# Kernel optimization log

Measured on AMD Instinct MI355X. Metric: run time of the kernel, lower is better.

The kernel has to match this reference:

```python
import jax, jax.numpy as jnp
import numpy as np

N = 100000   # nodes (single node type 'A')
C = 256      # hidden_channels
OUT = 128    # out_channels
E_RAND = 300000  # random edges; total E = N + E_RAND = 400000
LN_EPS = 1e-5


def _linear_params(key, in_c, out_c):
    kw, kb = jax.random.split(key)
    bound = 1.0 / np.sqrt(in_c)
    W = jax.random.uniform(kw, (out_c, in_c), minval=-bound, maxval=bound, dtype=jnp.float32)
    b = jax.random.uniform(kb, (out_c,), minval=-bound, maxval=bound, dtype=jnp.float32)
    return W, b


def _edges(key):
    # guarantee every node appears in both rows -> unique()/remap in the torch
    # code is the identity, so the subgraph equals the full graph
    k0, k1 = jax.random.split(key)
    base = jnp.arange(N, dtype=jnp.int64)
    row0 = jnp.concatenate([base, jax.random.randint(k0, (E_RAND,), 0, N, dtype=jnp.int64)])
    row1 = jnp.concatenate([base, jax.random.randint(k1, (E_RAND,), 0, N, dtype=jnp.int64)])
    return jnp.stack([row0, row1])


def setup_inputs() -> dict:
    key = jax.random.key(0)
    ks = jax.random.split(key, 12)
    x = jax.random.normal(ks[0], (N, C), dtype=jnp.float32)
    edge_index_r0 = _edges(ks[1])
    edge_index_r1 = _edges(ks[2])
    wl0, bl0 = _linear_params(ks[3], C, C)
    w00, b00 = _linear_params(ks[4], C, C)
    w10, b10 = _linear_params(ks[5], C, C)
    wl1, bl1 = _linear_params(ks[6], C, C)
    w01, b01 = _linear_params(ks[7], C, C)
    w11, b11 = _linear_params(ks[8], C, C)
    Wout, bout = _linear_params(ks[9], C, OUT)
    return dict(
        x=x, edge_index_r0=edge_index_r0, edge_index_r1=edge_index_r1,
        wl0=wl0, bl0=bl0, w00=w00, b00=b00, w10=w10, b10=b10,
        gate0=jnp.float32(0.5), lns0=jnp.ones((C,), jnp.float32), lnb0=jnp.zeros((C,), jnp.float32),
        wl1=wl1, bl1=bl1, w01=w01, b01=b01, w11=w11, b11=b11,
        gate1=jnp.float32(0.5), lns1=jnp.ones((C,), jnp.float32), lnb1=jnp.zeros((C,), jnp.float32),
        Wout=Wout, bout=bout,
    )


def _metapath_layer(x0, h, ei, wl, bl, w0, b0, w1, b1, gate, lns, lnb):
    n = h.shape[0]
    src, dst = ei[0], ei[1]
    # PyG flow='target_to_source', aggr='add': message x_j = h[edge_index[1]],
    # scatter-added at edge_index[0]
    agg = jax.ops.segment_sum(h[dst], src, num_segments=n)
    # original code normalizes by bincount of edge_index[1] (kept faithfully)
    deg = jax.ops.segment_sum(jnp.ones_like(dst, dtype=h.dtype), dst, num_segments=n)
    agg = agg / jnp.clip(deg, 1.0)[:, None]
    g = jax.nn.sigmoid(gate)
    out = (agg @ wl.T + bl) + (1.0 - g) * (h @ w0.T + b0) + g * (x0 @ w1.T + b1)
    out = jax.nn.relu(out)
    mu = out.mean(-1, keepdims=True)
    var = out.var(-1, keepdims=True)
    out = (out - mu) / jnp.sqrt(var + LN_EPS) * lns + lnb
    return out  # dropout is identity in eval mode


def reference(x, edge_index_r0, edge_index_r1,
              wl0, bl0, w00, b00, w10, b10, gate0, lns0, lnb0,
              wl1, bl1, w01, b01, w11, b11, gate1, lns1, lnb1,
              Wout, bout):
    x0 = jax.lax.stop_gradient(x)  # x0_dict is detached in the torch code
    h = x
    # metapath is processed in reverse: conv index 1 first, then conv index 0
    h = _metapath_layer(x0, h, edge_index_r1, wl1, bl1, w01, b01, w11, b11, gate1, lns1, lnb1)
    h = _metapath_layer(x0, h, edge_index_r0, wl0, bl0, w00, b00, w10, b10, gate0, lns0, lnb0)
    return h @ Wout.T + bout
```

## Files before the change

### kernel.cpp

```cpp
#include <hip/hip_runtime.h>

typedef unsigned short u16;
typedef unsigned int   u32;

typedef __attribute__((ext_vector_type(8))) __bf16 bf16x8;
typedef __attribute__((ext_vector_type(8))) unsigned short u16x8;
typedef __attribute__((ext_vector_type(4))) float  f32x4;

#define C      256
#define OUTC   128
#define LN_EPS 1e-5f

__device__ __forceinline__ float bf2f(u16 u) {
    u32 i = ((u32)u) << 16; float f; __builtin_memcpy(&f, &i, 4); return f;
}
__device__ __forceinline__ u16 f2bf(float f) {
    u32 i; __builtin_memcpy(&i, &f, 4);
    u32 r = (i + 0x7FFFu + ((i >> 16) & 1u)) >> 16;
    return (u16)r;
}
__device__ __forceinline__ void load_lds16(const void* g, void* l) {
    __builtin_amdgcn_global_load_lds((const __attribute__((address_space(1))) u32*)g,
                                     (__attribute__((address_space(3))) u32*)l, 16, 0, 0);
}
__device__ __forceinline__ int swz(int row) { return (row + (row >> 2)) & 3; }

#define PREP_BLK 1408
__global__ void prep_combo(const float* wl0, const float* w00, const float* w10,
                           const float* bl0, const float* b00, const float* b10,
                           const float* gate0,
                           const float* wl1, const float* w01, const float* w11,
                           const float* bl1, const float* b01, const float* b11,
                           const float* gate1,
                           const float* Wout, const float* x,
                           u16* __restrict__ WcatA, u16* __restrict__ WcatB,
                           u16* __restrict__ Woutb, float* __restrict__ bcat,
                           u16* __restrict__ xb, size_t n8)
{
    if (blockIdx.x >= PREP_BLK) {
        size_t i = ((size_t)(blockIdx.x - PREP_BLK) * 256 + threadIdx.x);
        if (i >= n8) return;
        const float* p = x + i * 8;
        float4 v0 = *(const float4*)p;
        float4 v1 = *(const float4*)(p + 4);
        u16x8 o;
        o[0] = f2bf(v0.x); o[1] = f2bf(v0.y); o[2] = f2bf(v0.z); o[3] = f2bf(v0.w);
        o[4] = f2bf(v1.x); o[5] = f2bf(v1.y); o[6] = f2bf(v1.z); o[7] = f2bf(v1.w);
        *(u16x8*)(xb + i * 8) = o;
        return;
    }
    int idx = blockIdx.x * 256 + threadIdx.x;
    float gA = 1.f / (1.f + expf(-gate1[0]));
    float gB = 1.f / (1.f + expf(-gate0[0]));
    if (idx < 256 * 512) {
        int n = idx >> 9, k = idx & 511;
        float v;
        if (k < 256) v = wl1[n * 256 + k];
        else         v = (1.f - gA) * w01[n * 256 + (k - 256)] + gA * w11[n * 256 + (k - 256)];
        WcatA[idx] = f2bf(v);
    } else if (idx < 256 * 512 + 256 * 768) {
        int j = idx - 256 * 512;
        int n = j / 768, k = j - n * 768;
        float v;
        if (k < 256)      v = wl0[n * 256 + k];
        else if (k < 512) v = (1.f - gB) * w00[n * 256 + (k - 256)];
        else              v = gB * w10[n * 256 + (k - 512)];
        WcatB[j] = f2bf(v);
    } else {
        int j = idx - (256 * 512 + 256 * 768);
        if (j < OUTC * C) Woutb[j] = f2bf(Wout[j]);
    }
    if (idx < 512) {
        int nn = idx & 255;
        if (idx < 256) bcat[idx] = bl1[nn] + (1.f - gA) * b01[nn] + gA * b11[nn];
        else           bcat[idx] = bl0[nn] + (1.f - gB) * b00[nn] + gB * b10[nn];
    }
}

__global__ void count_edges2(const int* __restrict__ ei1, const int* __restrict__ ei0,
                             int* __restrict__ cnt1, int* __restrict__ deg1,
                             int* __restrict__ cnt0, int* __restrict__ deg0,
                             int E, int Nn, int ebg)
{
    int b = blockIdx.x;
    const int* ei; int *cnt, *deg;
    if (b < ebg) { ei = ei1; cnt = cnt1; deg = deg1; }
    else         { b -= ebg; ei = ei0; cnt = cnt0; deg = deg0; }
    int idx = b * 256 + threadIdx.x;
    if (idx >= E) return;
    int s = ei[idx], d = ei[E + idx];
    if ((unsigned)s >= (unsigned)Nn || (unsigned)d >= (unsigned)Nn) return;
    atomicAdd(cnt + s, 1);
    atomicAdd(deg + d, 1);
}

__global__ void block_sums2(const int* __restrict__ cnt1, const int* __restrict__ cnt0,
                            int* __restrict__ parts1, int* __restrict__ parts0,
                            int n, int nblk)
{
    int b = blockIdx.x;
    const int* counts; int* partials;
    if (b < nblk) { counts = cnt1; partials = parts1; }
    else          { b -= nblk; counts = cnt0; partials = parts0; }
    int i = b * 256 + threadIdx.x;
    int v = (i < n) ? counts[i] : 0;
    #pragma unroll
    for (int off = 32; off; off >>= 1) v += __shfl_down(v, off, 64);
    __shared__ int ws[4];
    if ((threadIdx.x & 63) == 0) ws[threadIdx.x >> 6] = v;
    __syncthreads();
    if (threadIdx.x == 0) partials[b] = ws[0] + ws[1] + ws[2] + ws[3];
}

__global__ void scan_partials2(int* __restrict__ parts1, int* __restrict__ parts0, int nblk)
{
    int* partials = blockIdx.x ? parts0 : parts1;
    __shared__ int buf[1024];
    int tid = threadIdx.x;
    int v = (tid < nblk) ? partials[tid] : 0;
    buf[tid] = v; __syncthreads();
    for (int off = 1; off < 1024; off <<= 1) {
        int t = (tid >= off) ? buf[tid - off] : 0;
        __syncthreads();
        buf[tid] += t;
        __syncthreads();
    }
    if (tid < nblk) partials[tid] = buf[tid] - v;
}

__global__ void make_offsets2(int* __restrict__ cnt1, int* __restrict__ cnt0,
                              const int* __restrict__ parts1, const int* __restrict__ parts0,
                              int* __restrict__ off1a, int* __restrict__ off0a,
                              int n, int nblk)
{
    int b = blockIdx.x;
    int* counts_cursor; const int* partials; int* offsets;
    if (b < nblk) { counts_cursor = cnt1; partials = parts1; offsets = off1a; }
    else          { b -= nblk; counts_cursor = cnt0; partials = parts0; offsets = off0a; }
    __shared__ int buf[256];
    int i = b * 256 + threadIdx.x;
    int cnt = (i < n) ? counts_cursor[i] : 0;
    buf[threadIdx.x] = cnt; __syncthreads();
    for (int off = 1; off < 256; off <<= 1) {
        int t = (threadIdx.x >= off) ? buf[threadIdx.x - off] : 0;
        __syncthreads();
        buf[threadIdx.x] += t;
        __syncthreads();
    }
    int off = partials[b] + buf[threadIdx.x] - cnt;
    if (i < n) {
        offsets[i] = off;
        counts_cursor[i] = off;
        if (i == n - 1) offsets[n] = off + cnt;
    }
}

__global__ void fill_edges2(const int* __restrict__ ei1, const int* __restrict__ ei0,
                            int* __restrict__ cur1, int* __restrict__ cur0,
                            int* __restrict__ ed1, int* __restrict__ ed0,
                            int E, int Nn, int ebg)
{
    int b = blockIdx.x;
    const int* ei; int *cursor, *edgedst;
    if (b < ebg) { ei = ei1; cursor = cur1; edgedst = ed1; }
    else         { b -= ebg; ei = ei0; cursor = cur0; edgedst = ed0; }
    int idx = b * 256 + threadIdx.x;
    if (idx >= E) return;
    int s = ei[idx], d = ei[E + idx];
    if ((unsigned)s >= (unsigned)Nn || (unsigned)d >= (unsigned)Nn) return;
    int p = atomicAdd(cursor + s, 1);
    edgedst[p] = d;
}

__global__ __launch_bounds__(256) void gather_kernel(
    const int* __restrict__ offsets, const int* __restrict__ edgedst,
    const int* __restrict__ degcnt, const u16* __restrict__ h,
    u16* __restrict__ aggb, int Nn)
{
    int node = blockIdx.x * 4 + (threadIdx.x >> 6);
    if (node >= Nn) return;
    int lane = threadIdx.x & 63;
    int half = lane >> 5, l5 = lane & 31;
    int beg = offsets[node], end = offsets[node + 1];
    float a0[8] = {}, a1[8] = {};
    int p = beg;
    for (; p + 3 < end; p += 4) {
        int d0 = edgedst[p + half];
        int d1 = edgedst[p + 2 + half];
        u16x8 v0 = *(const u16x8*)(h + (size_t)d0 * C + l5 * 8);
        u16x8 v1 = *(const u16x8*)(h + (size_t)d1 * C + l5 * 8);
        #pragma unroll
        for (int j = 0; j < 8; ++j) { a0[j] += bf2f(v0[j]); a1[j] += bf2f(v1[j]); }
    }
    if (p + 1 < end) {
        int d0 = edgedst[p + half];
        u16x8 v0 = *(const u16x8*)(h + (size_t)d0 * C + l5 * 8);
        #pragma unroll
        for (int j = 0; j < 8; ++j) a0[j] += bf2f(v0[j]);
        p += 2;
    }
    if (p < end && half == 0) {
        int d0 = edgedst[p];
        u16x8 v0 = *(const u16x8*)(h + (size_t)d0 * C + l5 * 8);
        #pragma unroll
        for (int j = 0; j < 8; ++j) a1[j] += bf2f(v0[j]);
    }
    float inv = 1.0f / fmaxf((float)degcnt[node], 1.0f);
    u16x8 o;
    #pragma unroll
    for (int j = 0; j < 8; ++j) {
        float s = a0[j] + a1[j];
        s += __shfl_xor(s, 32);
        o[j] = f2bf(s * inv);
    }
    if (half == 0)
        *(u16x8*)(aggb + (size_t)node * C + l5 * 8) = o;
}

template <int NSEG>
__global__ __launch_bounds__(512, 2) void layer_gemm8(
    const u16* __restrict__ s0, const u16* __restrict__ s1, const u16* __restrict__ s2,
    const u16* __restrict__ W,
    const float* __restrict__ bcat,
    const float* __restrict__ lns, const float* __restrict__ lnb,
    u16* __restrict__ Hout, int Nnodes)
{
    constexpr int WK = NSEG * 256;
    constexpr int T  = NSEG * 4;

    extern __shared__ char smem[];
    u16*   A_e    = (u16*)smem;
    u16*   B_e    = (u16*)(smem + 65536);
    float* lnpart = (float*)(smem + 131072);

    const int tid  = threadIdx.x;
    const int wave = tid >> 6, lane = tid & 63;
    const int wave_m = wave & 1, wave_n = wave >> 1;
    const int q = lane >> 4, l15 = lane & 15;
    const int m0 = blockIdx.x * 256;

    size_t a_goff[2], b_goff[2];
    int ldso[2];
    #pragma unroll
    for (int i = 0; i < 2; ++i) {
        int o = i * 8192 + wave * 1024 + lane * 16;
        int g = o >> 7, slot = (o >> 4) & 7;
        int bc = slot ^ (g & 7);
        int r = 2 * g + (bc >> 2), c = bc & 3;
        int node = m0 + r; if (node >= Nnodes) node = Nnodes - 1;
        a_goff[i] = (size_t)node * C + c * 8;
        b_goff[i] = (size_t)r * WK + c * 8;
        ldso[i]   = i * 8192 + wave * 1024;
    }

    int aoffE[8], boffE[4];
    #pragma unroll
    for (int j = 0; j < 8; ++j) {
        int r = wave_m * 128 + j * 16 + l15;
        aoffE[j] = (r >> 1) * 64 + (((((r & 1) << 2) | q) ^ ((r >> 1) & 7)) << 3);
    }
    #pragma unroll
    for (int f = 0; f < 4; ++f) {
        int r = wave_n * 64 + f * 16 + l15;
        boffE[f] = (r >> 1) * 64 + (((((r & 1) << 2) | q) ^ ((r >> 1) & 7)) << 3);
    }

    f32x4 acc[8][4] = {};

    auto stA = [&](int buf, int kh, int t) {
        const u16* sp = (t < 4) ? s0 : ((NSEG == 2 || t < 8) ? s1 : s2);
        const u16* base = sp + ((t & 3) << 6) + (kh << 5);
        #pragma unroll
        for (int i = 0; i < 2; ++i)
            load_lds16(base + a_goff[i], (char*)A_e + buf * 32768 + kh * 16384 + ldso[i]);
    };
    auto stB = [&](int buf, int kh, int t) {
        const u16* base = W + (t << 6) + (kh << 5);
        #pragma unroll
        for (int i = 0; i < 2; ++i)
            load_lds16(base + b_goff[i], (char*)B_e + buf * 32768 + kh * 16384 + ldso[i]);
    };

#define LDA(DST, BASE, MH) \
    _Pragma("unroll") for (int j = 0; j < 4; ++j) \
        DST[j] = *(const bf16x8*)((BASE) + aoffE[(MH) * 4 + j]);
#define LDB(DST, BASE) \
    _Pragma("unroll") for (int f = 0; f < 4; ++f) \
        DST[f] = *(const bf16x8*)((BASE) + boffE[f]);
#define MFMA16(MH, AF, BF) \
    _Pragma("unroll") for (int j = 0; j < 4; ++j) \
        _Pragma("unroll") for (int f = 0; f < 4; ++f) \
            acc[(MH) * 4 + j][f] = __builtin_amdgcn_mfma_f32_16x16x32_bf16( \
                AF[j], BF[f], acc[(MH) * 4 + j][f], 0, 0, 0);
#define SBAR()  asm volatile("s_barrier" ::: "memory")

    stA(0, 0, 0); stB(0, 0, 0); stA(0, 1, 0); stB(0, 1, 0);

    int cur = 0;
    for (int t = 0; t < T - 1; ++t, cur ^= 1) {
        const u16* Ac = A_e + cur * 16384;
        const u16* Bc = B_e + cur * 16384;
        const int nxt = cur ^ 1;
        bf16x8 af[4], bfr[4];
        stA(nxt, 0, t + 1);
        asm volatile("s_waitcnt vmcnt(6)" ::: "memory");
        SBAR();
        __builtin_amdgcn_sched_barrier(0);
        LDB(bfr, Bc); LDA(af, Ac, 0);
        __builtin_amdgcn_s_setprio(1);
        MFMA16(0, af, bfr);
        __builtin_amdgcn_s_setprio(0);
        SBAR();
        LDA(af, Ac, 1);
        stB(nxt, 0, t + 1);
        SBAR();
        __builtin_amdgcn_s_setprio(1);
        MFMA16(1, af, bfr);
        __builtin_amdgcn_s_setprio(0);
        SBAR();
        stA(nxt, 1, t + 1);
        asm volatile("s_waitcnt vmcnt(6)" ::: "memory");
        SBAR();
        __builtin_amdgcn_sched_barrier(0);
        LDB(bfr, Bc + 8192); LDA(af, Ac + 8192, 0);
        __builtin_amdgcn_s_setprio(1);
        MFMA16(0, af, bfr);
        __builtin_amdgcn_s_setprio(0);
        SBAR();
        LDA(af, Ac + 8192, 1);
        stB(nxt, 1, t + 1);
        SBAR();
        __builtin_amdgcn_s_setprio(1);
        MFMA16(1, af, bfr);
        __builtin_amdgcn_s_setprio(0);
        SBAR();
    }
    {
        const u16* Ac = A_e + cur * 16384;
        const u16* Bc = B_e + cur * 16384;
        bf16x8 af[4], bfr[4];
        asm volatile("s_waitcnt vmcnt(4)" ::: "memory");
        SBAR();
        __builtin_amdgcn_sched_barrier(0);
        LDB(bfr, Bc); LDA(af, Ac, 0);
        __builtin_amdgcn_s_setprio(1);
        MFMA16(0, af, bfr);
        __builtin_amdgcn_s_setprio(0);
        SBAR();
        LDA(af, Ac, 1);
        SBAR();
        __builtin_amdgcn_s_setprio(1);
        MFMA16(1, af, bfr);
        __builtin_amdgcn_s_setprio(0);
        SBAR();
        asm volatile("s_waitcnt vmcnt(0)" ::: "memory");
        SBAR();
        __builtin_amdgcn_sched_barrier(0);
        LDB(bfr, Bc + 8192); LDA(af, Ac + 8192, 0);
        __builtin_amdgcn_s_setprio(1);
        MFMA16(0, af, bfr);
        __builtin_amdgcn_s_setprio(0);
        SBAR();
        LDA(af, Ac + 8192, 1);
        SBAR();
        __builtin_amdgcn_s_setprio(1);
        MFMA16(1, af, bfr);
        __builtin_amdgcn_s_setprio(0);
        SBAR();
    }

    float bias[4], lsc[4], lbi[4];
    #pragma unroll
    for (int f = 0; f < 4; ++f) {
        int n = wave_n * 64 + f * 16 + l15;
        bias[f] = bcat[n]; lsc[f] = lns[n]; lbi[f] = lnb[n];
    }
    #pragma unroll
    for (int t8 = 0; t8 < 8; ++t8)
        #pragma unroll
        for (int r = 0; r < 4; ++r) {
            float p = 0.f, pp = 0.f;
            #pragma unroll
            for (int f = 0; f < 4; ++f) {
                float v = acc[t8][f][r] + bias[f];
                v = fmaxf(v, 0.f);
                acc[t8][f][r] = v;
                p += v; pp += v * v;
            }
            #pragma unroll
            for (int off = 1; off < 16; off <<= 1) {
                p  += __shfl_xor(p,  off, 16);
                pp += __shfl_xor(pp, off, 16);
            }
            if (l15 == 0) {
                int row = wave_m * 128 + t8 * 16 + q * 4 + r;
                lnpart[row * 8 + wave_n * 2 + 0] = p;
                lnpart[row * 8 + wave_n * 2 + 1] = pp;
            }
        }
    __syncthreads();
    #pragma unroll
    for (int t8 = 0; t8 < 8; ++t8)
        #pragma unroll
        for (int r = 0; r < 4; ++r) {
            int row = wave_m * 128 + t8 * 16 + q * 4 + r;
            int node = m0 + row;
            if (node < Nnodes) {
                float S1 = lnpart[row * 8 + 0] + lnpart[row * 8 + 2]
                         + lnpart[row * 8 + 4] + lnpart[row * 8 + 6];
                float S2 = lnpart[row * 8 + 1] + lnpart[row * 8 + 3]
                         + lnpart[row * 8 + 5] + lnpart[row * 8 + 7];
                float mean = S1 * (1.f / 256.f);
                float var  = fmaxf(S2 * (1.f / 256.f) - mean * mean, 0.f);
                float rstd = rsqrtf(var + LN_EPS);
                u16* op = Hout + (size_t)node * C;
                #pragma unroll
                for (int f = 0; f < 4; ++f) {
                    int n = wave_n * 64 + f * 16 + l15;
                    op[n] = f2bf((acc[t8][f][r] - mean) * rstd * lsc[f] + lbi[f]);
                }
            }
        }
#undef LDA
#undef LDB
#undef MFMA16
#undef SBAR
}

__global__ __launch_bounds__(512, 4) void final_gemm(
    const u16* __restrict__ A, const u16* __restrict__ W,
    const float* __restrict__ bout, float* __restrict__ out, int Nnodes)
{
    __shared__ u16 Alds[2][128 * 32];
    __shared__ u16 Blds[2][128 * 32];

    const int tid = threadIdx.x;
    const int wave = tid >> 6, lane = tid & 63;
    const int wave_m = wave & 1, wave_n = wave >> 1;
    const int q = lane >> 4, l15 = lane & 15;
    const int m0 = blockIdx.x * 128;

    const int srow = (wave << 4) + (lane >> 2);
    int anode = m0 + srow; if (anode >= Nnodes) anode = Nnodes - 1;
    const int asc = (lane & 3) ^ swz(srow);
    const size_t a_goff = (size_t)anode * C + asc * 8;
    const int a_lo = wave << 9;

    const int bsc = (lane & 3) ^ swz(srow);
    const u16* bgp = W + srow * C + bsc * 8;
    const int b_lo = wave << 9;

    int aoff[4], boff[2];
    #pragma unroll
    for (int t = 0; t < 4; ++t) {
        int ar = wave_m * 64 + t * 16 + l15;
        aoff[t] = ar * 32 + ((q ^ swz(ar)) << 3);
    }
    #pragma unroll
    for (int f = 0; f < 2; ++f) {
        int br = wave_n * 32 + f * 16 + l15;
        boff[f] = br * 32 + ((q ^ swz(br)) << 3);
    }

    f32x4 acc[4][2] = {};

    auto stage = [&](int b, int kt) {
        int k0 = kt << 5;
        load_lds16(A + a_goff + k0, &Alds[b][a_lo]);
        load_lds16(bgp + k0, &Blds[b][b_lo]);
    };
    auto compute = [&](const u16* __restrict__ Ab, const u16* __restrict__ Bb) {
        bf16x8 af[4], bfr[2];
        #pragma unroll
        for (int t = 0; t < 4; ++t) af[t]  = *(const bf16x8*)(Ab + aoff[t]);
        #pragma unroll
        for (int f = 0; f < 2; ++f) bfr[f] = *(const bf16x8*)(Bb + boff[f]);
        #pragma unroll
        for (int t = 0; t < 4; ++t)
            #pragma unroll
            for (int f = 0; f < 2; ++f)
                acc[t][f] = __builtin_amdgcn_mfma_f32_16x16x32_bf16(af[t], bfr[f], acc[t][f], 0, 0, 0);
    };

    stage(0, 0);
    stage(1, 1);
    for (int kt = 0; kt < 6; kt += 2) {
        asm volatile("s_waitcnt vmcnt(2)" ::: "memory");
        __builtin_amdgcn_s_barrier();
        __builtin_amdgcn_sched_barrier(0);
        compute(&Alds[0][0], &Blds[0][0]);
        __builtin_amdgcn_sched_barrier(0);
        __builtin_amdgcn_s_barrier();
        stage(0, kt + 2);
        asm volatile("s_waitcnt vmcnt(2)" ::: "memory");
        __builtin_amdgcn_s_barrier();
        __builtin_amdgcn_sched_barrier(0);
        compute(&Alds[1][0], &Blds[1][0]);
        __builtin_amdgcn_sched_barrier(0);
        __builtin_amdgcn_s_barrier();
        stage(1, kt + 3);
    }
    asm volatile("s_waitcnt vmcnt(2)" ::: "memory");
    __builtin_amdgcn_s_barrier();
    __builtin_amdgcn_sched_barrier(0);
    compute(&Alds[0][0], &Blds[0][0]);
    asm volatile("s_waitcnt vmcnt(0)" ::: "memory");
    __builtin_amdgcn_s_barrier();
    __builtin_amdgcn_sched_barrier(0);
    compute(&Alds[1][0], &Blds[1][0]);

    float bias[2];
    #pragma unroll
    for (int f = 0; f < 2; ++f) bias[f] = bout[wave_n * 32 + f * 16 + l15];
    #pragma unroll
    for (int t = 0; t < 4; ++t)
        #pragma unroll
        for (int r = 0; r < 4; ++r) {
            int row = wave_m * 64 + t * 16 + q * 4 + r;
            int node = m0 + row;
            if (node < Nnodes) {
                float* op = out + (size_t)node * OUTC;
                #pragma unroll
                for (int f = 0; f < 2; ++f) {
                    int n = wave_n * 32 + f * 16 + l15;
                    op[n] = acc[t][f][r] + bias[f];
                }
            }
        }
}

extern "C" void kernel_launch(void* const* d_in, const int* in_sizes, int n_in,
                              void* d_out, int out_size, void* d_ws, size_t ws_size,
                              hipStream_t stream)
{
    const float* x    = (const float*)d_in[0];
    const int*   ei0  = (const int*)d_in[1];
    const int*   ei1  = (const int*)d_in[2];
    const float* wl0  = (const float*)d_in[3];
    const float* bl0  = (const float*)d_in[4];
    const float* w00  = (const float*)d_in[5];
    const float* b00  = (const float*)d_in[6];
    const float* w10  = (const float*)d_in[7];
    const float* b10  = (const float*)d_in[8];
    const float* gate0= (const float*)d_in[9];
    const float* lns0 = (const float*)d_in[10];
    const float* lnb0 = (const float*)d_in[11];
    const float* wl1  = (const float*)d_in[12];
    const float* bl1  = (const float*)d_in[13];
    const float* w01  = (const float*)d_in[14];
    const float* b01  = (const float*)d_in[15];
    const float* w11  = (const float*)d_in[16];
    const float* b11  = (const float*)d_in[17];
    const float* gate1= (const float*)d_in[18];
    const float* lns1 = (const float*)d_in[19];
    const float* lnb1 = (const float*)d_in[20];
    const float* Wout = (const float*)d_in[21];
    const float* bout = (const float*)d_in[22];

    const int N = in_sizes[0] / C;
    const int E = in_sizes[1] / 2;

    char* w = (char*)d_ws;
    u16*   WcatA = (u16*)w;   w += (size_t)256 * 512 * 2;
    u16*   WcatB = (u16*)w;   w += (size_t)256 * 768 * 2;
    u16*   Woutb = (u16*)w;   w += (size_t)OUTC * C * 2;
    float* bcat  = (float*)w; w += 4096;
    int*   cnt1  = (int*)w;   w += (size_t)N * 4;
    int*   deg1  = (int*)w;   w += (size_t)N * 4;
    int*   cnt0  = (int*)w;   w += (size_t)N * 4;
    int*   deg0  = (int*)w;   w += (size_t)N * 4;
    int*   off1  = (int*)w;   w += (((size_t)(N + 1) * 4) + 255) & ~255ull;
    int*   off0  = (int*)w;   w += (((size_t)(N + 1) * 4) + 255) & ~255ull;
    int*   parts1= (int*)w;   w += 4096;
    int*   parts0= (int*)w;   w += 4096;
    int*   ed1   = (int*)w;   w += (size_t)E * 4;
    int*   ed0   = (int*)w;   w += (size_t)E * 4;
    u16*   xb    = (u16*)w;   w += (size_t)N * C * 2;
    u16*   aggb  = (u16*)w;   w += (size_t)N * C * 2;
    u16*   h1    = (u16*)w;   w += (size_t)N * C * 2;

    const int eb_grid = (E + 255) / 256;
    const int nblk    = (N + 255) / 256;
    const int gt_grid = (N + 3) / 4;
    const int gm_grid = (N + 127) / 128;
    const int gm8     = (N + 255) / 256;
    const size_t n8   = (size_t)N * C / 8;
    const int xc_blk  = (int)((n8 + 255) / 256);
    const size_t lds8 = 139264;
    u16* h2 = (u16*)d_out;

    hipMemsetAsync(cnt1, 0, (size_t)4 * N * 4, stream);
    prep_combo<<<PREP_BLK + xc_blk, 256, 0, stream>>>(
        wl0, w00, w10, bl0, b00, b10, gate0,
        wl1, w01, w11, bl1, b01, b11, gate1,
        Wout, x, WcatA, WcatB, Woutb, bcat, xb, n8);

    count_edges2 <<<2 * eb_grid, 256, 0, stream>>>(ei1, ei0, cnt1, deg1, cnt0, deg0, E, N, eb_grid);
    block_sums2  <<<2 * nblk, 256, 0, stream>>>(cnt1, cnt0, parts1, parts0, N, nblk);
    scan_partials2<<<2, 1024, 0, stream>>>(parts1, parts0, nblk);
    make_offsets2<<<2 * nblk, 256, 0, stream>>>(cnt1, cnt0, parts1, parts0, off1, off0, N, nblk);
    fill_edges2  <<<2 * eb_grid, 256, 0, stream>>>(ei1, ei0, cnt1, cnt0, ed1, ed0, E, N, eb_grid);

    gather_kernel<<<gt_grid, 256, 0, stream>>>(off1, ed1, deg1, xb, aggb, N);
    layer_gemm8<2><<<gm8, 512, lds8, stream>>>(aggb, xb, nullptr, WcatA, bcat,
                                               lns1, lnb1, h1, N);

    gather_kernel<<<gt_grid, 256, 0, stream>>>(off0, ed0, deg0, h1, aggb, N);
    layer_gemm8<3><<<gm8, 512, lds8, stream>>>(aggb, h1, xb, WcatB, bcat + C,
                                               lns0, lnb0, h2, N);

    final_gemm<<<gm_grid, 512, 0, stream>>>(h2, Woutb, bout, (float*)d_out, N);
}
```

Before: 541.0 us.

## Fuse output projection into second layer GEMM and trim main-loop barriers

The second layer GEMM now writes its layer-normalized bf16 rows into swizzled LDS and runs the 256x128 output projection in the epilogue, reading Wout straight from global memory. This removes the separate final_gemm launch and the round trip of h2 through global memory. The main K loop also issues A and B stages together and waits once per half, which drops several s_barriers. In exchange the fused epilogue adds serial MFMA work after the main loop, and the fewer barriers assume LDS reads and writes do not race.

```diff
diff --git a/kernel.cpp b/kernel.cpp
--- a/kernel.cpp
+++ b/kernel.cpp
@@ -23,7 +23,6 @@
     __builtin_amdgcn_global_load_lds((const __attribute__((address_space(1))) u32*)g,
                                      (__attribute__((address_space(3))) u32*)l, 16, 0, 0);
 }
-__device__ __forceinline__ int swz(int row) { return (row + (row >> 2)) & 3; }
 
 #define PREP_BLK 1408
 __global__ void prep_combo(const float* wl0, const float* w00, const float* w10,
@@ -217,13 +216,15 @@
         *(u16x8*)(aggb + (size_t)node * C + l5 * 8) = o;
 }
 
-template <int NSEG>
+template <int NSEG, bool FUSE>
 __global__ __launch_bounds__(512, 2) void layer_gemm8(
     const u16* __restrict__ s0, const u16* __restrict__ s1, const u16* __restrict__ s2,
     const u16* __restrict__ W,
     const float* __restrict__ bcat,
     const float* __restrict__ lns, const float* __restrict__ lnb,
-    u16* __restrict__ Hout, int Nnodes)
+    u16* __restrict__ Hout,
+    const u16* __restrict__ WoutB, const float* __restrict__ boutp,
+    float* __restrict__ outp, int Nnodes)
 {
     constexpr int WK = NSEG * 256;
     constexpr int T  = NSEG * 4;
@@ -232,6 +233,7 @@
     u16*   A_e    = (u16*)smem;
     u16*   B_e    = (u16*)(smem + 65536);
     float* lnpart = (float*)(smem + 131072);
+    u16*   h2l    = (u16*)smem;
 
     const int tid  = threadIdx.x;
     const int wave = tid >> 6, lane = tid & 63;
@@ -302,34 +304,28 @@
         const u16* Bc = B_e + cur * 16384;
         const int nxt = cur ^ 1;
         bf16x8 af[4], bfr[4];
-        stA(nxt, 0, t + 1);
-        asm volatile("s_waitcnt vmcnt(6)" ::: "memory");
+        stA(nxt, 0, t + 1); stB(nxt, 0, t + 1);
+        asm volatile("s_waitcnt vmcnt(8)" ::: "memory");
         SBAR();
         __builtin_amdgcn_sched_barrier(0);
         LDB(bfr, Bc); LDA(af, Ac, 0);
         __builtin_amdgcn_s_setprio(1);
         MFMA16(0, af, bfr);
         __builtin_amdgcn_s_setprio(0);
-        SBAR();
         LDA(af, Ac, 1);
-        stB(nxt, 0, t + 1);
-        SBAR();
         __builtin_amdgcn_s_setprio(1);
         MFMA16(1, af, bfr);
         __builtin_amdgcn_s_setprio(0);
         SBAR();
-        stA(nxt, 1, t + 1);
-        asm volatile("s_waitcnt vmcnt(6)" ::: "memory");
+        stA(nxt, 1, t + 1); stB(nxt, 1, t + 1);
+        asm volatile("s_waitcnt vmcnt(8)" ::: "memory");
         SBAR();
         __builtin_amdgcn_sched_barrier(0);
         LDB(bfr, Bc + 8192); LDA(af, Ac + 8192, 0);
         __builtin_amdgcn_s_setprio(1);
         MFMA16(0, af, bfr);
         __builtin_amdgcn_s_setprio(0);
-        SBAR();
         LDA(af, Ac + 8192, 1);
-        stB(nxt, 1, t + 1);
-        SBAR();
         __builtin_amdgcn_s_setprio(1);
         MFMA16(1, af, bfr);
         __builtin_amdgcn_s_setprio(0);
@@ -346,9 +342,7 @@
         __builtin_amdgcn_s_setprio(1);
         MFMA16(0, af, bfr);
         __builtin_amdgcn_s_setprio(0);
-        SBAR();
         LDA(af, Ac, 1);
-        SBAR();
         __builtin_amdgcn_s_setprio(1);
         MFMA16(1, af, bfr);
         __builtin_amdgcn_s_setprio(0);
@@ -360,13 +354,10 @@
         __builtin_amdgcn_s_setprio(1);
         MFMA16(0, af, bfr);
         __builtin_amdgcn_s_setprio(0);
-        SBAR();
         LDA(af, Ac + 8192, 1);
-        SBAR();
         __builtin_amdgcn_s_setprio(1);
         MFMA16(1, af, bfr);
         __builtin_amdgcn_s_setprio(0);
-        SBAR();
     }
 
     float bias[4], lsc[4], lbi[4];
@@ -405,14 +396,21 @@
         for (int r = 0; r < 4; ++r) {
             int row = wave_m * 128 + t8 * 16 + q * 4 + r;
             int node = m0 + row;
-            if (node < Nnodes) {
-                float S1 = lnpart[row * 8 + 0] + lnpart[row * 8 + 2]
-                         + lnpart[row * 8 + 4] + lnpart[row * 8 + 6];
-                float S2 = lnpart[row * 8 + 1] + lnpart[row * 8 + 3]
-                         + lnpart[row * 8 + 5] + lnpart[row * 8 + 7];
-                float mean = S1 * (1.f / 256.f);
-                float var  = fmaxf(S2 * (1.f / 256.f) - mean * mean, 0.f);
-                float rstd = rsqrtf(var + LN_EPS);
+            float S1 = lnpart[row * 8 + 0] + lnpart[row * 8 + 2]
+                     + lnpart[row * 8 + 4] + lnpart[row * 8 + 6];
+            float S2 = lnpart[row * 8 + 1] + lnpart[row * 8 + 3]
+                     + lnpart[row * 8 + 5] + lnpart[row * 8 + 7];
+            float mean = S1 * (1.f / 256.f);
+            float var  = fmaxf(S2 * (1.f / 256.f) - mean * mean, 0.f);
+            float rstd = rsqrtf(var + LN_EPS);
+            if constexpr (FUSE) {
+                #pragma unroll
+                for (int f = 0; f < 4; ++f) {
+                    int n = wave_n * 64 + f * 16 + l15;
+                    u16 hv = f2bf((acc[t8][f][r] - mean) * rstd * lsc[f] + lbi[f]);
+                    h2l[row * 256 + (((n >> 3) ^ (row & 7)) << 3) + (n & 7)] = hv;
+                }
+            } else if (node < Nnodes) {
                 u16* op = Hout + (size_t)node * C;
                 #pragma unroll
                 for (int f = 0; f < 4; ++f) {
@@ -421,112 +419,49 @@
                 }
             }
         }
+
+    if constexpr (FUSE) {
+        __syncthreads();
+        f32x4 acc2[8][2] = {};
+        for (int kt = 0; kt < 8; ++kt) {
+            bf16x8 bw[2];
+            #pragma unroll
+            for (int f = 0; f < 2; ++f) {
+                int n = wave_n * 32 + f * 16 + l15;
+                bw[f] = *(const bf16x8*)(WoutB + (size_t)n * 256 + kt * 32 + q * 8);
+            }
+            #pragma unroll
+            for (int t8 = 0; t8 < 8; ++t8) {
+                int row = wave_m * 128 + t8 * 16 + l15;
+                bf16x8 a = *(const bf16x8*)(h2l + row * 256
+                                            + ((((kt << 2) | q) ^ (row & 7)) << 3));
+                #pragma unroll
+                for (int f = 0; f < 2; ++f)
+                    acc2[t8][f] = __builtin_amdgcn_mfma_f32_16x16x32_bf16(
+                        a, bw[f], acc2[t8][f], 0, 0, 0);
+            }
+        }
+        float b2[2];
+        #pragma unroll
+        for (int f = 0; f < 2; ++f) b2[f] = boutp[wave_n * 32 + f * 16 + l15];
+        #pragma unroll
+        for (int t8 = 0; t8 < 8; ++t8)
+            #pragma unroll
+            for (int r = 0; r < 4; ++r) {
+                int row = wave_m * 128 + t8 * 16 + q * 4 + r;
+                int node = m0 + row;
+                if (node < Nnodes) {
+                    float* op = outp + (size_t)node * OUTC;
+                    #pragma unroll
+                    for (int f = 0; f < 2; ++f)
+                        op[wave_n * 32 + f * 16 + l15] = acc2[t8][f][r] + b2[f];
+                }
+            }
+    }
 #undef LDA
 #undef LDB
 #undef MFMA16
 #undef SBAR
-}
-
-__global__ __launch_bounds__(512, 4) void final_gemm(
-    const u16* __restrict__ A, const u16* __restrict__ W,
-    const float* __restrict__ bout, float* __restrict__ out, int Nnodes)
-{
-    __shared__ u16 Alds[2][128 * 32];
-    __shared__ u16 Blds[2][128 * 32];
-
-    const int tid = threadIdx.x;
-    const int wave = tid >> 6, lane = tid & 63;
-    const int wave_m = wave & 1, wave_n = wave >> 1;
-    const int q = lane >> 4, l15 = lane & 15;
-    const int m0 = blockIdx.x * 128;
-
-    const int srow = (wave << 4) + (lane >> 2);
-    int anode = m0 + srow; if (anode >= Nnodes) anode = Nnodes - 1;
-    const int asc = (lane & 3) ^ swz(srow);
-    const size_t a_goff = (size_t)anode * C + asc * 8;
-    const int a_lo = wave << 9;
-
-    const int bsc = (lane & 3) ^ swz(srow);
-    const u16* bgp = W + srow * C + bsc * 8;
-    const int b_lo = wave << 9;
-
-    int aoff[4], boff[2];
-    #pragma unroll
-    for (int t = 0; t < 4; ++t) {
-        int ar = wave_m * 64 + t * 16 + l15;
-        aoff[t] = ar * 32 + ((q ^ swz(ar)) << 3);
-    }
-    #pragma unroll
-    for (int f = 0; f < 2; ++f) {
-        int br = wave_n * 32 + f * 16 + l15;
-        boff[f] = br * 32 + ((q ^ swz(br)) << 3);
-    }
-
-    f32x4 acc[4][2] = {};
-
-    auto stage = [&](int b, int kt) {
-        int k0 = kt << 5;
-        load_lds16(A + a_goff + k0, &Alds[b][a_lo]);
-        load_lds16(bgp + k0, &Blds[b][b_lo]);
-    };
-    auto compute = [&](const u16* __restrict__ Ab, const u16* __restrict__ Bb) {
-        bf16x8 af[4], bfr[2];
-        #pragma unroll
-        for (int t = 0; t < 4; ++t) af[t]  = *(const bf16x8*)(Ab + aoff[t]);
-        #pragma unroll
-        for (int f = 0; f < 2; ++f) bfr[f] = *(const bf16x8*)(Bb + boff[f]);
-        #pragma unroll
-        for (int t = 0; t < 4; ++t)
-            #pragma unroll
-            for (int f = 0; f < 2; ++f)
-                acc[t][f] = __builtin_amdgcn_mfma_f32_16x16x32_bf16(af[t], bfr[f], acc[t][f], 0, 0, 0);
-    };
-
-    stage(0, 0);
-    stage(1, 1);
-    for (int kt = 0; kt < 6; kt += 2) {
-        asm volatile("s_waitcnt vmcnt(2)" ::: "memory");
-        __builtin_amdgcn_s_barrier();
-        __builtin_amdgcn_sched_barrier(0);
-        compute(&Alds[0][0], &Blds[0][0]);
-        __builtin_amdgcn_sched_barrier(0);
-        __builtin_amdgcn_s_barrier();
-        stage(0, kt + 2);
-        asm volatile("s_waitcnt vmcnt(2)" ::: "memory");
-        __builtin_amdgcn_s_barrier();
-        __builtin_amdgcn_sched_barrier(0);
-        compute(&Alds[1][0], &Blds[1][0]);
-        __builtin_amdgcn_sched_barrier(0);
-        __builtin_amdgcn_s_barrier();
-        stage(1, kt + 3);
-    }
-    asm volatile("s_waitcnt vmcnt(2)" ::: "memory");
-    __builtin_amdgcn_s_barrier();
-    __builtin_amdgcn_sched_barrier(0);
-    compute(&Alds[0][0], &Blds[0][0]);
-    asm volatile("s_waitcnt vmcnt(0)" ::: "memory");
-    __builtin_amdgcn_s_barrier();
-    __builtin_amdgcn_sched_barrier(0);
-    compute(&Alds[1][0], &Blds[1][0]);
-
-    float bias[2];
-    #pragma unroll
-    for (int f = 0; f < 2; ++f) bias[f] = bout[wave_n * 32 + f * 16 + l15];
-    #pragma unroll
-    for (int t = 0; t < 4; ++t)
-        #pragma unroll
-        for (int r = 0; r < 4; ++r) {
-            int row = wave_m * 64 + t * 16 + q * 4 + r;
-            int node = m0 + row;
-            if (node < Nnodes) {
-                float* op = out + (size_t)node * OUTC;
-                #pragma unroll
-                for (int f = 0; f < 2; ++f) {
-                    int n = wave_n * 32 + f * 16 + l15;
-                    op[n] = acc[t][f][r] + bias[f];
-                }
-            }
-        }
 }
 
 extern "C" void kernel_launch(void* const* d_in, const int* in_sizes, int n_in,
@@ -582,12 +517,10 @@
     const int eb_grid = (E + 255) / 256;
     const int nblk    = (N + 255) / 256;
     const int gt_grid = (N + 3) / 4;
-    const int gm_grid = (N + 127) / 128;
     const int gm8     = (N + 255) / 256;
     const size_t n8   = (size_t)N * C / 8;
     const int xc_blk  = (int)((n8 + 255) / 256);
     const size_t lds8 = 139264;
-    u16* h2 = (u16*)d_out;
 
     hipMemsetAsync(cnt1, 0, (size_t)4 * N * 4, stream);
     prep_combo<<<PREP_BLK + xc_blk, 256, 0, stream>>>(
@@ -602,12 +535,12 @@
     fill_edges2  <<<2 * eb_grid, 256, 0, stream>>>(ei1, ei0, cnt1, cnt0, ed1, ed0, E, N, eb_grid);
 
     gather_kernel<<<gt_grid, 256, 0, stream>>>(off1, ed1, deg1, xb, aggb, N);
-    layer_gemm8<2><<<gm8, 512, lds8, stream>>>(aggb, xb, nullptr, WcatA, bcat,
-                                               lns1, lnb1, h1, N);
+    layer_gemm8<2, false><<<gm8, 512, lds8, stream>>>(aggb, xb, nullptr, WcatA, bcat,
+                                                      lns1, lnb1, h1,
+                                                      nullptr, nullptr, nullptr, N);
 
     gather_kernel<<<gt_grid, 256, 0, stream>>>(off0, ed0, deg0, h1, aggb, N);
-    layer_gemm8<3><<<gm8, 512, lds8, stream>>>(aggb, h1, xb, WcatB, bcat + C,
-                                               lns0, lnb0, h2, N);
-
-    final_gemm<<<gm_grid, 512, 0, stream>>>(h2, Woutb, bout, (float*)d_out, N);
-}
+    layer_gemm8<3, true><<<gm8, 512, lds8, stream>>>(aggb, h1, xb, WcatB, bcat + C,
+                                                     lns0, lnb0, nullptr,
+                                                     Woutb, bout, (float*)d_out, N);
+}
```

Result: faster. 528.6 us (-2.3%).
